# Performance work log

Hardware: AMD Instinct MI355X
Metric: run time of the kernel (lower is better)

Reference implementation:

```python
import jax, jax.numpy as jnp
import numpy as np
from jax import lax

B, ROWS, COLS, K, LATENT = 8, 1536, 16, 32, 16
EPS_REG = 0.01  # torchsort regularization_strength
BIG = 1e30


def setup_inputs() -> dict:
    key = jax.random.key(0)
    ks = jax.random.split(key, 12)
    def w(k, shape):
        return (jax.random.normal(k, shape, jnp.float32) / np.sqrt(shape[0])).astype(jnp.float32)
    return {
        "table": jax.random.uniform(ks[0], (B, ROWS, COLS), jnp.float32),
        "enc_w1": w(ks[1], (COLS, 32)), "enc_b1": 0.01 * jax.random.normal(ks[2], (32,), jnp.float32),
        "enc_w2": w(ks[3], (32, 64)),   "enc_b2": 0.01 * jax.random.normal(ks[4], (64,), jnp.float32),
        "mean_w": w(ks[5], (64, LATENT)), "mean_b": 0.01 * jax.random.normal(ks[6], (LATENT,), jnp.float32),
        "dec_w1": w(ks[7], (LATENT, 32)), "dec_b1": 0.01 * jax.random.normal(ks[8], (32,), jnp.float32),
        "dec_w2": w(ks[9], (32, COLS)),   "dec_b2": 0.01 * jax.random.normal(ks[10], (COLS,), jnp.float32),
        "labels": jax.random.randint(ks[11], (ROWS,), 0, K, jnp.int32),
        "BlockSize": 64,
        "current_epoch": 0,
        "baseline": 0,
    }


def _soft_rank_l2(s, eps):
    # Exact soft_rank (Blondel et al. / torchsort, l2 reg, ascending):
    # project s/eps onto permutahedron of (n,...,1).
    n = s.shape[0]
    x = s / eps
    perm = jnp.argsort(-x)            # descending sort
    xs = x[perm]
    w = jnp.arange(n, 0, -1, dtype=x.dtype)
    # dual = non-increasing isotonic fit of y = xs - w == -iso_inc(-(xs - w))
    y = -(xs - w)
    S = jnp.concatenate([jnp.zeros((1,), x.dtype), jnp.cumsum(y)])
    idx = jnp.arange(n)
    length = jnp.maximum(idx[None, :] - idx[:, None] + 1, 1).astype(x.dtype)
    A = (S[1:][None, :] - S[:n][:, None]) / length           # mean(y[j..k])  [j,k]
    A = jnp.where(idx[None, :] >= idx[:, None], A, BIG)
    Bm = lax.cummin(A, axis=1, reverse=True)                  # min_{k>=i} A[j,k]
    Cm = lax.cummax(Bm, axis=0)                               # max_{j<=i} ...
    iso_inc = jnp.diagonal(Cm)
    dual = -iso_inc
    primal = xs - dual
    inv = jnp.argsort(perm)
    return primal[inv]


def _forward(table, enc_w1, enc_b1, enc_w2, enc_b2, mean_w, mean_b,
             dec_w1, dec_b1, dec_w2, dec_b2, labels, BlockSize):
    b = table.shape[0]
    # VAE (autoencoder path; z = latent mean)
    h = jax.nn.relu(table @ enc_w1 + enc_b1)
    h = jax.nn.relu(h @ enc_w2 + enc_b2)
    z = h @ mean_w + mean_b                                   # [B, rows, 16]
    r = jax.nn.relu(z @ dec_w1 + dec_b1)
    recon = jax.nn.relu(r @ dec_w2 + dec_b2)
    loss = jnp.mean((recon - table) ** 2)
    # clustering scores (labels fixed from batch 0, shared across batch)
    onehot = jax.nn.one_hot(labels, K, dtype=z.dtype)         # [rows, K]
    counts = jnp.maximum(onehot.sum(0), 1.0)                  # [K]
    centers = jnp.einsum('brd,rk->bkd', z, onehot) / counts[None, :, None]
    center_data = centers[:, labels, :]                       # gather back [B, rows, 16]
    d2 = jnp.mean((z - center_data) ** 2, axis=-1)            # [B, rows]
    mn = d2.min(axis=1, keepdims=True); mx = d2.max(axis=1, keepdims=True)
    d2 = (d2 - mn) / (mx - mn)
    scores = d2 + labels.astype(z.dtype)[None, :]
    # training branch
    smn = scores.min(axis=1, keepdims=True); smx = scores.max(axis=1, keepdims=True)
    scaled = (scores - smn) / (smx - smn) * jnp.asarray(b, z.dtype)  # * len(table)
    ranks = jax.vmap(lambda s: _soft_rank_l2(s, EPS_REG))(scaled)
    rank_idx = jnp.argsort(jnp.argsort(scores, axis=1), axis=1) // BlockSize + 1
    rows = table.shape[1]
    return (ranks.reshape(b, rows, 1), rank_idx.reshape(b, rows, 1),
            scores.reshape(b, rows, 1), loss)


def reference(table, enc_w1, enc_b1, enc_w2, enc_b2, mean_w, mean_b,
              dec_w1, dec_b1, dec_w2, dec_b2, labels, BlockSize,
              current_epoch, baseline):
    return _forward(table, enc_w1, enc_b1, enc_w2, enc_b2, mean_w, mean_b,
                    dec_w1, dec_b1, dec_w2, dec_b2, labels, BlockSize)
```

## Files before the change

### kernel.cpp

```cpp
#include <hip/hip_runtime.h>

#define BATCH 8
#define ROWS 1536
#define KCLS 32
#define NTOT (BATCH*ROWS)
#define ELEMS (NTOT*16)
#define SSTRIDE 3073
#define BIGF 1.0e30f

enum : int {
  WS_Z     = 0,
  WS_X     = WS_Z + NTOT*16,
  WS_XS    = WS_X + NTOT,
  WS_S     = WS_XS + NTOT,
  WS_DESC  = WS_S + BATCH*SSTRIDE,
  WS_ASCP  = WS_DESC + NTOT,
  WS_DSCP  = WS_ASCP + 4*NTOT,
  WS_GPART = WS_DSCP + 4*NTOT,
  WS_LOSSP = WS_GPART + BATCH*96*512,
  WS_D2    = WS_LOSSP + 768,
  WS_MM    = WS_D2 + NTOT,
};
#define WS_CPART WS_GPART

#define LW1  0
#define LB1  512
#define LW2  544
#define LB2  2592
#define LMW  2656
#define LMB  3680
#define LDW1 3696
#define LDB1 4208
#define LDW2 4240
#define LDB2 4752
#define LTOT 4768

#define AX   0
#define AH1  16
#define AH2  48
#define AZ   112
#define AR1  128
#define AREC 144
#define ASTRIDE 164

#define RPB 16

template<int IN_BASE, int IN_N, int OUT_BASE, int OUT_PW, int OUT_TOT,
         int WOFF, int BOFF, bool RELU>
__device__ __forceinline__ void layerw(float* __restrict__ act,
                                       const float* __restrict__ wsh,
                                       int lrow, int fway)
{
  const int o0 = fway * OUT_PW;
  float acc[OUT_PW];
#pragma unroll
  for (int j = 0; j < OUT_PW; ++j) acc[j] = wsh[BOFF + o0 + j];

  const float4* arow = reinterpret_cast<const float4*>(&act[lrow*ASTRIDE + IN_BASE]);
#pragma unroll 2
  for (int i4 = 0; i4 < IN_N/4; ++i4) {
    float4 sv = arow[i4];
    float svx[4];
    svx[0] = sv.x; svx[1] = sv.y; svx[2] = sv.z; svx[3] = sv.w;
#pragma unroll
    for (int u = 0; u < 4; ++u) {
      const float s = svx[u];
      const float* wp = &wsh[WOFF + (i4*4 + u)*OUT_TOT + o0];
      if constexpr (OUT_PW == 1) {
        acc[0] = fmaf(s, wp[0], acc[0]);
      } else if constexpr (OUT_PW == 2) {
        float2 w = *reinterpret_cast<const float2*>(wp);
        acc[0] = fmaf(s, w.x, acc[0]);
        acc[1] = fmaf(s, w.y, acc[1]);
      } else {
#pragma unroll
        for (int q = 0; q < OUT_PW/4; ++q) {
          float4 w = reinterpret_cast<const float4*>(wp)[q];
          acc[q*4+0] = fmaf(s, w.x, acc[q*4+0]);
          acc[q*4+1] = fmaf(s, w.y, acc[q*4+1]);
          acc[q*4+2] = fmaf(s, w.z, acc[q*4+2]);
          acc[q*4+3] = fmaf(s, w.w, acc[q*4+3]);
        }
      }
    }
  }
  float* orow = &act[lrow*ASTRIDE + OUT_BASE + o0];
  if constexpr (OUT_PW == 1) {
    orow[0] = RELU ? fmaxf(acc[0], 0.f) : acc[0];
  } else if constexpr (OUT_PW == 2) {
    float2 v;
    v.x = RELU ? fmaxf(acc[0], 0.f) : acc[0];
    v.y = RELU ? fmaxf(acc[1], 0.f) : acc[1];
    *reinterpret_cast<float2*>(orow) = v;
  } else {
#pragma unroll
    for (int q = 0; q < OUT_PW/4; ++q) {
      float4 v;
      v.x = RELU ? fmaxf(acc[q*4+0], 0.f) : acc[q*4+0];
      v.y = RELU ? fmaxf(acc[q*4+1], 0.f) : acc[q*4+1];
      v.z = RELU ? fmaxf(acc[q*4+2], 0.f) : acc[q*4+2];
      v.w = RELU ? fmaxf(acc[q*4+3], 0.f) : acc[q*4+3];
      reinterpret_cast<float4*>(orow)[q] = v;
    }
  }
}

__global__ __launch_bounds__(256, 4) void k1_ae(
    const float* __restrict__ table,
    const float* __restrict__ w1, const float* __restrict__ b1,
    const float* __restrict__ w2, const float* __restrict__ b2,
    const float* __restrict__ mw, const float* __restrict__ mb,
    const float* __restrict__ dw1, const float* __restrict__ db1,
    const float* __restrict__ dw2, const float* __restrict__ db2,
    const int* __restrict__ labels,
    float* __restrict__ ws)
{
  const int tid  = threadIdx.x;
  const int lrow = tid & (RPB-1);
  const int fway = tid >> 4;
  const int blk  = blockIdx.x;
  const int b    = blk / 96;
  const int ch   = blk % 96;

  __shared__ float wsh[LTOT];
  __shared__ float act[RPB * ASTRIDE];
  __shared__ int   lbl[RPB];
  __shared__ float lred[4];

  {
    float4* d4 = reinterpret_cast<float4*>(wsh);
#define CPY(off, src, nf4) \
    { const float4* p = reinterpret_cast<const float4*>(src); \
      for (int t = tid; t < (nf4); t += 256) d4[(off)/4 + t] = p[t]; }
    CPY(LW1,  w1,  128) CPY(LB1,  b1,  8)  CPY(LW2,  w2,  512)
    CPY(LB2,  b2,  16)  CPY(LMW,  mw,  256) CPY(LMB,  mb,  4)
    CPY(LDW1, dw1, 128) CPY(LDB1, db1, 8)  CPY(LDW2, dw2, 128)
    CPY(LDB2, db2, 4)
#undef CPY
    if (tid < RPB) lbl[tid] = labels[ch * RPB + tid];
    if (tid < RPB*4) {
      const float4 v = reinterpret_cast<const float4*>(table)[blk*(RPB*4) + tid];
      reinterpret_cast<float4*>(act)[(tid >> 2)*(ASTRIDE/4) + (tid & 3)] = v;
    }
  }
  __syncthreads();

  layerw<AX,  16, AH1, 2, 32, LW1,  LB1,  true >(act, wsh, lrow, fway);
  __syncthreads();
  layerw<AH1, 32, AH2, 4, 64, LW2,  LB2,  true >(act, wsh, lrow, fway);
  __syncthreads();
  layerw<AH2, 64, AZ,  1, 16, LMW,  LMB,  false>(act, wsh, lrow, fway);
  __syncthreads();

  if (tid < RPB*4) {
    const float4 zv =
      reinterpret_cast<const float4*>(act)[(tid >> 2)*(ASTRIDE/4) + (AZ/4) + (tid & 3)];
    reinterpret_cast<float4*>(ws + WS_Z)[blk*(RPB*4) + tid] = zv;
  }

  layerw<AZ,  16, AR1, 2, 32, LDW1, LDB1, true >(act, wsh, lrow, fway);
  __syncthreads();
  layerw<AR1, 32, AREC,1, 16, LDW2, LDB2, true >(act, wsh, lrow, fway);
  __syncthreads();

  {
    const float d = act[lrow*ASTRIDE + AREC + fway] - act[lrow*ASTRIDE + AX + fway];
    float ls = d * d;
    for (int off = 32; off > 0; off >>= 1) ls += __shfl_down(ls, off);
    if ((tid & 63) == 0) lred[tid >> 6] = ls;
    __syncthreads();
    if (tid == 0) ws[WS_LOSSP + blk] = (lred[0] + lred[1]) + (lred[2] + lred[3]);
  }

  {
    float a0 = 0.f, a1 = 0.f;
    const int d0 = tid & 15, k0 = tid >> 4;
    const int k1c = k0 + 16;
#pragma unroll
    for (int rr = 0; rr < RPB; ++rr) {
      const int lb = lbl[rr];
      const float zv = act[rr*ASTRIDE + AZ + d0];
      a0 += (lb == k0)  ? zv : 0.f;
      a1 += (lb == k1c) ? zv : 0.f;
    }
    ws[WS_CPART + (b*96 + ch)*512 + tid]       = a0;
    ws[WS_CPART + (b*96 + ch)*512 + 256 + tid] = a1;
  }
}

__global__ __launch_bounds__(256) void kcd2(const int* __restrict__ labels,
                                            float* __restrict__ ws,
                                            float* __restrict__ out)
{
  const int bi = blockIdx.x;
  const int b = bi / 6, ib = bi % 6;
  const int tid = threadIdx.x;

  __shared__ int   cnt[KCLS];
  __shared__ int   lbls[256];
  __shared__ float cent[512];
  __shared__ float rmn[256], rmx[256];

  if (tid < KCLS) cnt[tid] = 0;
  __syncthreads();
#pragma unroll
  for (int c = 0; c < 6; ++c) {
    const int lb = labels[c*256 + tid];
    if (c == ib) lbls[tid] = lb;
    atomicAdd(&cnt[lb], 1);
  }
  __syncthreads();

#pragma unroll
  for (int e = tid; e < 512; e += 256) {
    float s = 0.f;
#pragma unroll 8
    for (int c = 0; c < 96; ++c) s += ws[WS_CPART + (b*96 + c)*512 + e];
    const int cn = cnt[e >> 4] > 1 ? cnt[e >> 4] : 1;
    cent[e] = s / (float)cn;
  }
  __syncthreads();

  const int r = ib*256 + tid;
  {
    const int lb = lbls[tid];
    const float4* zp = reinterpret_cast<const float4*>(ws + WS_Z + (b*ROWS + r)*16);
    const float4* cp = reinterpret_cast<const float4*>(&cent[lb*16]);
    float s = 0.f;
#pragma unroll
    for (int q = 0; q < 4; ++q) {
      float4 zv = zp[q], cv = cp[q];
      float d0 = zv.x - cv.x, d1 = zv.y - cv.y, d2_ = zv.z - cv.z, d3 = zv.w - cv.w;
      s += d0*d0 + d1*d1 + d2_*d2_ + d3*d3;
    }
    const float dv = s / 16.f;
    ws[WS_D2 + b*ROWS + r] = dv;
    rmn[tid] = dv; rmx[tid] = dv;
  }
  __syncthreads();
  for (int off = 128; off > 0; off >>= 1) {
    if (tid < off) {
      rmn[tid] = fminf(rmn[tid], rmn[tid + off]);
      rmx[tid] = fmaxf(rmx[tid], rmx[tid + off]);
    }
    __syncthreads();
  }
  if (tid == 0) {
    ws[WS_MM + bi*2]     = rmn[0];
    ws[WS_MM + bi*2 + 1] = rmx[0];
  }

  if (bi == 0) {
    __syncthreads();
    rmn[tid] = ws[WS_LOSSP + tid] + ws[WS_LOSSP + 256 + tid] + ws[WS_LOSSP + 512 + tid];
    __syncthreads();
    for (int off = 128; off > 0; off >>= 1) {
      if (tid < off) rmn[tid] += rmn[tid + off];
      __syncthreads();
    }
    if (tid == 0) out[3*NTOT] = rmn[0] / (float)ELEMS;
  }
}

__global__ __launch_bounds__(256) void kcount(const int* __restrict__ labels,
                                              float* __restrict__ ws,
                                              float* __restrict__ out)
{
  const int bi = blockIdx.x;
  const int jb = bi & 3, rb = (bi >> 2) % 6, b = bi / 24;
  const int tid = threadIdx.x;

  alignas(16) __shared__ float s_l[ROWS];
  alignas(16) __shared__ float x_l[ROWS];
  __shared__ float rmn[256], rmx[256];

  float mn = 3.0e38f, mx = -3.0e38f;
#pragma unroll
  for (int c = 0; c < 6; ++c) {
    mn = fminf(mn, ws[WS_MM + (b*6 + c)*2]);
    mx = fmaxf(mx, ws[WS_MM + (b*6 + c)*2 + 1]);
  }

  float tmn = 3.0e38f, tmx = -3.0e38f;
#pragma unroll
  for (int c = 0; c < 6; ++c) {
    const int r = c*256 + tid;
    const float sc = (ws[WS_D2 + b*ROWS + r] - mn) / (mx - mn) + (float)labels[r];
    s_l[r] = sc;
    if (jb == 0 && c == rb) out[2*NTOT + b*ROWS + r] = sc;
    tmn = fminf(tmn, sc); tmx = fmaxf(tmx, sc);
  }
  rmn[tid] = tmn; rmx[tid] = tmx;
  __syncthreads();
  for (int off = 128; off > 0; off >>= 1) {
    if (tid < off) {
      rmn[tid] = fminf(rmn[tid], rmn[tid + off]);
      rmx[tid] = fmaxf(rmx[tid], rmx[tid + off]);
    }
    __syncthreads();
  }
  const float smn = rmn[0], smx = rmx[0];

#pragma unroll
  for (int c = 0; c < 6; ++c) {
    const int r = c*256 + tid;
    const float scl = (s_l[r] - smn) / (smx - smn) * 8.0f;
    const float xv = scl / 0.01f;
    x_l[r] = xv;
    if (jb == 0 && c == rb) ws[WS_X + b*ROWS + r] = xv;
  }
  __syncthreads();

  const int r0 = rb*256 + tid;
  const float si = s_l[r0], xi = x_l[r0];
  int asc = 0, dsc = 0;
  const int j0 = jb*384;
  const float4* s4p = reinterpret_cast<const float4*>(&s_l[j0]);
  const float4* x4p = reinterpret_cast<const float4*>(&x_l[j0]);
#pragma unroll 4
  for (int kk = 0; kk < 96; ++kk) {
    const float4 s4 = s4p[kk];
    const float4 x4 = x4p[kk];
    const int j = j0 + kk*4;
    asc += (s4.x < si || (s4.x == si && j   < r0)) ? 1 : 0;
    asc += (s4.y < si || (s4.y == si && j+1 < r0)) ? 1 : 0;
    asc += (s4.z < si || (s4.z == si && j+2 < r0)) ? 1 : 0;
    asc += (s4.w < si || (s4.w == si && j+3 < r0)) ? 1 : 0;
    dsc += (x4.x > xi || (x4.x == xi && j   < r0)) ? 1 : 0;
    dsc += (x4.y > xi || (x4.y == xi && j+1 < r0)) ? 1 : 0;
    dsc += (x4.z > xi || (x4.z == xi && j+2 < r0)) ? 1 : 0;
    dsc += (x4.w > xi || (x4.w == xi && j+3 < r0)) ? 1 : 0;
  }
  int* wsi = reinterpret_cast<int*>(ws);
  wsi[WS_ASCP + jb*NTOT + b*ROWS + r0] = asc;
  wsi[WS_DSCP + jb*NTOT + b*ROWS + r0] = dsc;
}

__global__ __launch_bounds__(256) void k67(const int* __restrict__ bsp,
                                           float* __restrict__ ws,
                                           float* __restrict__ out)
{
  const int b = blockIdx.x, tid = threadIdx.x;
  const int lane = tid & 63, wav = tid >> 6;
  __shared__ float xs_l[ROWS];
  __shared__ float wtot[4];
  const int* wsi = reinterpret_cast<const int*>(ws);
  int* wsw = reinterpret_cast<int*>(ws);
  const int BS = *bsp;
#pragma unroll
  for (int c = 0; c < 6; ++c) {
    const int r = c*256 + tid;
    const int idx = b*ROWS + r;
    int asc = 0, dsc = 0;
#pragma unroll
    for (int jb = 0; jb < 4; ++jb) {
      asc += wsi[WS_ASCP + jb*NTOT + idx];
      dsc += wsi[WS_DSCP + jb*NTOT + idx];
    }
    out[NTOT + idx] = (float)(asc / BS + 1);
    wsw[WS_DESC + idx] = dsc;
    xs_l[dsc] = ws[WS_X + idx];
  }
  __syncthreads();
  const int base = tid * 6;
  float y[6], own = 0.f;
#pragma unroll
  for (int u = 0; u < 6; ++u) {
    ws[WS_XS + b*ROWS + base + u] = xs_l[base + u];
    y[u] = (float)(ROWS - (base + u)) - xs_l[base + u];
    own += y[u];
  }
  float v = own;
#pragma unroll
  for (int d = 1; d < 64; d <<= 1) {
    float o = __shfl_up(v, d);
    if (lane >= d) v += o;
  }
  if (lane == 63) wtot[wav] = v;
  __syncthreads();
  float wpre = 0.f;
  for (int w = 0; w < wav; ++w) wpre += wtot[w];
  float run = wpre + (v - own);
  float* S = ws + WS_S + b*SSTRIDE;
#pragma unroll
  for (int u = 0; u < 6; ++u) { S[base + u] = run; run += y[u]; }
  if (tid == 255) S[ROWS] = run;
#pragma unroll
  for (int u = 0; u < 6; ++u) S[ROWS + 1 + tid*6 + u] = BIGF;
}

__global__ __launch_bounds__(256) void k8a(float* __restrict__ ws)
{
  const int bi = blockIdx.x;
  const int c = bi & 7, ib = (bi >> 3) % 6, b = bi / 48;
  const int tid = threadIdx.x;
  __shared__ float Sseg[448];
  __shared__ float invl[192];
  const float* S = ws + WS_S + b*SSTRIDE;
  const int ibase = ib*256;
  const int segbase = ibase + c*192 + 1;
  Sseg[tid] = S[segbase + tid];
  if (tid < 192) {
    Sseg[256 + tid] = S[segbase + 256 + tid];
    invl[tid] = 1.0f / (float)(c*192 + tid + 1);
  }
  __syncthreads();
  const int i = ibase + tid;
  const float Si = S[i];
  float gm = 3.0e38f;
#pragma unroll 8
  for (int k = 0; k < 192; ++k)
    gm = fminf(gm, (Sseg[tid + k] - Si) * invl[k]);
  ws[WS_GPART + (b*8 + c)*ROWS + i] = gm;
}

__global__ __launch_bounds__(768) void k8b(float* __restrict__ ws,
                                           float* __restrict__ out)
{
  const int b = blockIdx.x, tid = threadIdx.x;
  const int lane = tid & 63, wav = tid >> 6;
  __shared__ float g[ROWS];
  __shared__ float wtot[12];
  for (int t = tid; t < ROWS; t += 768) {
    float gm = 3.0e38f;
#pragma unroll
    for (int c = 0; c < 8; ++c)
      gm = fminf(gm, ws[WS_GPART + (b*8 + c)*ROWS + t]);
    g[t] = gm;
  }
  __syncthreads();
  const float a = g[2*tid], cc = g[2*tid + 1];
  float v = fmaxf(a, cc);
#pragma unroll
  for (int d = 1; d < 64; d <<= 1) {
    float o = __shfl_up(v, d);
    if (lane >= d) v = fmaxf(v, o);
  }
  if (lane == 63) wtot[wav] = v;
  __syncthreads();
  float wpre = -3.0e38f;
  for (int w = 0; w < wav; ++w) wpre = fmaxf(wpre, wtot[w]);
  float lex = __shfl_up(v, 1);
  if (lane == 0) lex = -3.0e38f;
  const float excl = fmaxf(wpre, lex);
  const float i0 = fmaxf(excl, a);
  const float i1 = fmaxf(i0, cc);
  g[2*tid] = i0; g[2*tid + 1] = i1;
  __syncthreads();
  const float* xs = ws + WS_XS + b*ROWS;
  const int* desc = reinterpret_cast<const int*>(ws) + WS_DESC + b*ROWS;
  for (int t = tid; t < ROWS; t += 768) {
    const int dr = desc[t];
    out[b*ROWS + t] = xs[dr] + g[dr];
  }
}

extern "C" void kernel_launch(void* const* d_in, const int* in_sizes, int n_in,
                              void* d_out, int out_size, void* d_ws, size_t ws_size,
                              hipStream_t stream) {
  const float* table = (const float*)d_in[0];
  const float* w1  = (const float*)d_in[1];
  const float* b1  = (const float*)d_in[2];
  const float* w2  = (const float*)d_in[3];
  const float* b2  = (const float*)d_in[4];
  const float* mw  = (const float*)d_in[5];
  const float* mb  = (const float*)d_in[6];
  const float* dw1 = (const float*)d_in[7];
  const float* db1 = (const float*)d_in[8];
  const float* dw2 = (const float*)d_in[9];
  const float* db2 = (const float*)d_in[10];
  const int* labels = (const int*)d_in[11];
  const int* bsp    = (const int*)d_in[12];
  float* out = (float*)d_out;
  float* ws  = (float*)d_ws;

  k1_ae<<<768, 256, 0, stream>>>(table, w1, b1, w2, b2, mw, mb, dw1, db1, dw2, db2, labels, ws);
  kcd2<<<48, 256, 0, stream>>>(labels, ws, out);
  kcount<<<192, 256, 0, stream>>>(labels, ws, out);
  k67<<<8, 256, 0, stream>>>(bsp, ws, out);
  k8a<<<384, 256, 0, stream>>>(ws);
  k8b<<<8, 768, 0, stream>>>(ws, out);
}
```

Baseline: 69.99 us.

## Compute per-batch scores and scaled ranks once in a 1024-thread block kernel

```diff
diff --git a/kernel.cpp b/kernel.cpp
--- a/kernel.cpp
+++ b/kernel.cpp
@@ -18,8 +18,6 @@
   WS_DSCP  = WS_ASCP + 4*NTOT,
   WS_GPART = WS_DSCP + 4*NTOT,
   WS_LOSSP = WS_GPART + BATCH*96*512,
-  WS_D2    = WS_LOSSP + 768,
-  WS_MM    = WS_D2 + NTOT,
 };
 #define WS_CPART WS_GPART
 
@@ -188,83 +186,117 @@
   }
 }
 
-__global__ __launch_bounds__(256) void kcd2(const int* __restrict__ labels,
-                                            float* __restrict__ ws,
-                                            float* __restrict__ out)
-{
-  const int bi = blockIdx.x;
-  const int b = bi / 6, ib = bi % 6;
+__global__ __launch_bounds__(1024) void kmid8(const int* __restrict__ labels,
+                                              float* __restrict__ ws,
+                                              float* __restrict__ out)
+{
+  const int b = blockIdx.x;
   const int tid = threadIdx.x;
-
-  __shared__ int   cnt[KCLS];
-  __shared__ int   lbls[256];
-  __shared__ float cent[512];
-  __shared__ float rmn[256], rmx[256];
+  const int lane = tid & 63, wav = tid >> 6;
+
+  __shared__ int cnt[KCLS];
+  alignas(16) __shared__ float cent[512];
+  alignas(16) __shared__ float part[1024];
+  __shared__ float wr1[16], wr2[16];
 
   if (tid < KCLS) cnt[tid] = 0;
   __syncthreads();
-#pragma unroll
-  for (int c = 0; c < 6; ++c) {
-    const int lb = labels[c*256 + tid];
-    if (c == ib) lbls[tid] = lb;
-    atomicAdd(&cnt[lb], 1);
-  }
-  __syncthreads();
-
-#pragma unroll
-  for (int e = tid; e < 512; e += 256) {
+  const int lb1 = labels[tid];
+  const int lb2 = (tid < 512) ? labels[1024 + tid] : 0;
+  atomicAdd(&cnt[lb1], 1);
+  if (tid < 512) atomicAdd(&cnt[lb2], 1);
+
+  {
+    const int e = tid & 511, g = tid >> 9;
+    const float* cp = ws + WS_CPART + (b*96 + g*48)*512 + e;
     float s = 0.f;
 #pragma unroll 8
-    for (int c = 0; c < 96; ++c) s += ws[WS_CPART + (b*96 + c)*512 + e];
-    const int cn = cnt[e >> 4] > 1 ? cnt[e >> 4] : 1;
-    cent[e] = s / (float)cn;
-  }
-  __syncthreads();
-
-  const int r = ib*256 + tid;
-  {
-    const int lb = lbls[tid];
+    for (int c = 0; c < 48; ++c) s += cp[c*512];
+    part[tid] = s;
+  }
+  __syncthreads();
+  if (tid < 512) {
+    const int cn = cnt[tid >> 4] > 1 ? cnt[tid >> 4] : 1;
+    cent[tid] = (part[tid] + part[tid + 512]) / (float)cn;
+  }
+
+  if (b == 0) {
+    float ls = (tid < 768) ? ws[WS_LOSSP + tid] : 0.f;
+    for (int off = 32; off > 0; off >>= 1) ls += __shfl_down(ls, off);
+    if (lane == 0) wr1[wav] = ls;
+  }
+  __syncthreads();
+  if (b == 0 && tid == 0) {
+    float L = 0.f;
+#pragma unroll
+    for (int w = 0; w < 16; ++w) L += wr1[w];
+    out[3*NTOT] = L / (float)ELEMS;
+  }
+
+  auto d2row = [&](int r, int lb) -> float {
     const float4* zp = reinterpret_cast<const float4*>(ws + WS_Z + (b*ROWS + r)*16);
-    const float4* cp = reinterpret_cast<const float4*>(&cent[lb*16]);
+    const float4* cq = reinterpret_cast<const float4*>(&cent[lb*16]);
     float s = 0.f;
 #pragma unroll
     for (int q = 0; q < 4; ++q) {
-      float4 zv = zp[q], cv = cp[q];
+      float4 zv = zp[q], cv = cq[q];
       float d0 = zv.x - cv.x, d1 = zv.y - cv.y, d2_ = zv.z - cv.z, d3 = zv.w - cv.w;
       s += d0*d0 + d1*d1 + d2_*d2_ + d3*d3;
     }
-    const float dv = s / 16.f;
-    ws[WS_D2 + b*ROWS + r] = dv;
-    rmn[tid] = dv; rmx[tid] = dv;
-  }
-  __syncthreads();
-  for (int off = 128; off > 0; off >>= 1) {
-    if (tid < off) {
-      rmn[tid] = fminf(rmn[tid], rmn[tid + off]);
-      rmx[tid] = fmaxf(rmx[tid], rmx[tid + off]);
-    }
-    __syncthreads();
-  }
-  if (tid == 0) {
-    ws[WS_MM + bi*2]     = rmn[0];
-    ws[WS_MM + bi*2 + 1] = rmx[0];
-  }
-
-  if (bi == 0) {
-    __syncthreads();
-    rmn[tid] = ws[WS_LOSSP + tid] + ws[WS_LOSSP + 256 + tid] + ws[WS_LOSSP + 512 + tid];
-    __syncthreads();
-    for (int off = 128; off > 0; off >>= 1) {
-      if (tid < off) rmn[tid] += rmn[tid + off];
-      __syncthreads();
-    }
-    if (tid == 0) out[3*NTOT] = rmn[0] / (float)ELEMS;
-  }
-}
-
-__global__ __launch_bounds__(256) void kcount(const int* __restrict__ labels,
-                                              float* __restrict__ ws,
-                                              float* __restrict__ out)
+    return s / 16.f;
+  };
+  const float dv1 = d2row(tid, lb1);
+  const float dv2 = (tid < 512) ? d2row(1024 + tid, lb2) : 0.f;
+
+  {
+    float mn = (tid < 512) ? fminf(dv1, dv2) : dv1;
+    float mx = (tid < 512) ? fmaxf(dv1, dv2) : dv1;
+    for (int off = 32; off > 0; off >>= 1) {
+      mn = fminf(mn, __shfl_down(mn, off));
+      mx = fmaxf(mx, __shfl_down(mx, off));
+    }
+    if (lane == 0) { wr1[wav] = mn; wr2[wav] = mx; }
+  }
+  __syncthreads();
+  float mn = 3.0e38f, mx = -3.0e38f;
+#pragma unroll
+  for (int w = 0; w < 16; ++w) {
+    mn = fminf(mn, wr1[w]); mx = fmaxf(mx, wr2[w]);
+  }
+  __syncthreads();
+
+  const float sc1 = (dv1 - mn) / (mx - mn) + (float)lb1;
+  const float sc2 = (tid < 512) ? (dv2 - mn) / (mx - mn) + (float)lb2 : 0.f;
+  out[2*NTOT + b*ROWS + tid] = sc1;
+  if (tid < 512) out[2*NTOT + b*ROWS + 1024 + tid] = sc2;
+  {
+    float smn = (tid < 512) ? fminf(sc1, sc2) : sc1;
+    float smx = (tid < 512) ? fmaxf(sc1, sc2) : sc1;
+    for (int off = 32; off > 0; off >>= 1) {
+      smn = fminf(smn, __shfl_down(smn, off));
+      smx = fmaxf(smx, __shfl_down(smx, off));
+    }
+    if (lane == 0) { wr1[wav] = smn; wr2[wav] = smx; }
+  }
+  __syncthreads();
+  float smn = 3.0e38f, smx = -3.0e38f;
+#pragma unroll
+  for (int w = 0; w < 16; ++w) {
+    smn = fminf(smn, wr1[w]); smx = fmaxf(smx, wr2[w]);
+  }
+
+  {
+    const float x1 = (sc1 - smn) / (smx - smn) * 8.0f / 0.01f;
+    ws[WS_X + b*ROWS + tid] = x1;
+    if (tid < 512) {
+      const float x2 = (sc2 - smn) / (smx - smn) * 8.0f / 0.01f;
+      ws[WS_X + b*ROWS + 1024 + tid] = x2;
+    }
+  }
+}
+
+__global__ __launch_bounds__(256) void kcount(float* __restrict__ ws,
+                                              const float* __restrict__ out)
 {
   const int bi = blockIdx.x;
   const int jb = bi & 3, rb = (bi >> 2) % 6, b = bi / 24;
@@ -272,42 +304,12 @@
 
   alignas(16) __shared__ float s_l[ROWS];
   alignas(16) __shared__ float x_l[ROWS];
-  __shared__ float rmn[256], rmx[256];
-
-  float mn = 3.0e38f, mx = -3.0e38f;
-#pragma unroll
-  for (int c = 0; c < 6; ++c) {
-    mn = fminf(mn, ws[WS_MM + (b*6 + c)*2]);
-    mx = fmaxf(mx, ws[WS_MM + (b*6 + c)*2 + 1]);
-  }
-
-  float tmn = 3.0e38f, tmx = -3.0e38f;
+
 #pragma unroll
   for (int c = 0; c < 6; ++c) {
     const int r = c*256 + tid;
-    const float sc = (ws[WS_D2 + b*ROWS + r] - mn) / (mx - mn) + (float)labels[r];
-    s_l[r] = sc;
-    if (jb == 0 && c == rb) out[2*NTOT + b*ROWS + r] = sc;
-    tmn = fminf(tmn, sc); tmx = fmaxf(tmx, sc);
-  }
-  rmn[tid] = tmn; rmx[tid] = tmx;
-  __syncthreads();
-  for (int off = 128; off > 0; off >>= 1) {
-    if (tid < off) {
-      rmn[tid] = fminf(rmn[tid], rmn[tid + off]);
-      rmx[tid] = fmaxf(rmx[tid], rmx[tid + off]);
-    }
-    __syncthreads();
-  }
-  const float smn = rmn[0], smx = rmx[0];
-
-#pragma unroll
-  for (int c = 0; c < 6; ++c) {
-    const int r = c*256 + tid;
-    const float scl = (s_l[r] - smn) / (smx - smn) * 8.0f;
-    const float xv = scl / 0.01f;
-    x_l[r] = xv;
-    if (jb == 0 && c == rb) ws[WS_X + b*ROWS + r] = xv;
+    s_l[r] = out[2*NTOT + b*ROWS + r];
+    x_l[r] = ws[WS_X + b*ROWS + r];
   }
   __syncthreads();
 
@@ -475,8 +477,8 @@
   float* ws  = (float*)d_ws;
 
   k1_ae<<<768, 256, 0, stream>>>(table, w1, b1, w2, b2, mw, mb, dw1, db1, dw2, db2, labels, ws);
-  kcd2<<<48, 256, 0, stream>>>(labels, ws, out);
-  kcount<<<192, 256, 0, stream>>>(labels, ws, out);
+  kmid8<<<8, 1024, 0, stream>>>(labels, ws, out);
+  kcount<<<192, 256, 0, stream>>>(ws, out);
   k67<<<8, 256, 0, stream>>>(bsp, ws, out);
   k8a<<<384, 256, 0, stream>>>(ws);
   k8b<<<8, 768, 0, stream>>>(ws, out);
```

Measured after the change: 61.93 us. 1.13x faster.

## Split centroid reduction into parallel kernel and derive descending ranks from scores

Applied to the files above, without the earlier changes.

```diff
diff --git a/kernel.cpp b/kernel.cpp
--- a/kernel.cpp
+++ b/kernel.cpp
@@ -10,8 +10,7 @@
 
 enum : int {
   WS_Z     = 0,
-  WS_X     = WS_Z + NTOT*16,
-  WS_XS    = WS_X + NTOT,
+  WS_XS    = WS_Z + NTOT*16,
   WS_S     = WS_XS + NTOT,
   WS_DESC  = WS_S + BATCH*SSTRIDE,
   WS_ASCP  = WS_DESC + NTOT,
@@ -20,6 +19,8 @@
   WS_LOSSP = WS_GPART + BATCH*96*512,
   WS_D2    = WS_LOSSP + 768,
   WS_MM    = WS_D2 + NTOT,
+  WS_CPAR2 = WS_MM + 96,
+  WS_CNT   = WS_CPAR2 + BATCH*8*512,
 };
 #define WS_CPART WS_GPART
 
@@ -188,55 +189,80 @@
   }
 }
 
-__global__ __launch_bounds__(256) void kcd2(const int* __restrict__ labels,
+__global__ __launch_bounds__(512) void kcen(const int* __restrict__ labels,
                                             float* __restrict__ ws,
                                             float* __restrict__ out)
+{
+  const int bi = blockIdx.x;
+  const int b = bi >> 3, g = bi & 7;
+  const int tid = threadIdx.x;
+
+  const float* cp = ws + WS_CPART + (b*96 + g*12)*512 + tid;
+  float s = 0.f;
+#pragma unroll
+  for (int c = 0; c < 12; ++c) s += cp[c*512];
+  ws[WS_CPAR2 + (b*8 + g)*512 + tid] = s;
+
+  if (bi == 0) {
+    __shared__ int icnt[KCLS];
+    __shared__ float red[512];
+    if (tid < KCLS) icnt[tid] = 0;
+    __syncthreads();
+    atomicAdd(&icnt[labels[tid]], 1);
+    atomicAdd(&icnt[labels[512 + tid]], 1);
+    atomicAdd(&icnt[labels[1024 + tid]], 1);
+    red[tid] = ws[WS_LOSSP + tid] + ((tid < 256) ? ws[WS_LOSSP + 512 + tid] : 0.f);
+    __syncthreads();
+    for (int off = 256; off > 0; off >>= 1) {
+      if (tid < off) red[tid] += red[tid + off];
+      __syncthreads();
+    }
+    if (tid == 0) out[3*NTOT] = red[0] / (float)ELEMS;
+    if (tid < KCLS) reinterpret_cast<int*>(ws)[WS_CNT + tid] = icnt[tid];
+  }
+}
+
+__global__ __launch_bounds__(256) void kd2(const int* __restrict__ labels,
+                                           float* __restrict__ ws)
 {
   const int bi = blockIdx.x;
   const int b = bi / 6, ib = bi % 6;
   const int tid = threadIdx.x;
 
-  __shared__ int   cnt[KCLS];
-  __shared__ int   lbls[256];
   __shared__ float cent[512];
   __shared__ float rmn[256], rmx[256];
-
-  if (tid < KCLS) cnt[tid] = 0;
-  __syncthreads();
-#pragma unroll
-  for (int c = 0; c < 6; ++c) {
-    const int lb = labels[c*256 + tid];
-    if (c == ib) lbls[tid] = lb;
-    atomicAdd(&cnt[lb], 1);
-  }
-  __syncthreads();
-
-#pragma unroll
-  for (int e = tid; e < 512; e += 256) {
-    float s = 0.f;
-#pragma unroll 8
-    for (int c = 0; c < 96; ++c) s += ws[WS_CPART + (b*96 + c)*512 + e];
-    const int cn = cnt[e >> 4] > 1 ? cnt[e >> 4] : 1;
-    cent[e] = s / (float)cn;
+  __shared__ int ci[KCLS];
+
+  if (tid < KCLS) ci[tid] = reinterpret_cast<const int*>(ws)[WS_CNT + tid];
+  float s1 = 0.f, s2 = 0.f;
+#pragma unroll
+  for (int g = 0; g < 8; ++g) {
+    s1 += ws[WS_CPAR2 + (b*8 + g)*512 + tid];
+    s2 += ws[WS_CPAR2 + (b*8 + g)*512 + 256 + tid];
+  }
+  __syncthreads();
+  {
+    int cn1 = ci[tid >> 4];         cn1 = cn1 > 1 ? cn1 : 1;
+    int cn2 = ci[(tid + 256) >> 4]; cn2 = cn2 > 1 ? cn2 : 1;
+    cent[tid]       = s1 / (float)cn1;
+    cent[tid + 256] = s2 / (float)cn2;
   }
   __syncthreads();
 
   const int r = ib*256 + tid;
-  {
-    const int lb = lbls[tid];
-    const float4* zp = reinterpret_cast<const float4*>(ws + WS_Z + (b*ROWS + r)*16);
-    const float4* cp = reinterpret_cast<const float4*>(&cent[lb*16]);
-    float s = 0.f;
-#pragma unroll
-    for (int q = 0; q < 4; ++q) {
-      float4 zv = zp[q], cv = cp[q];
-      float d0 = zv.x - cv.x, d1 = zv.y - cv.y, d2_ = zv.z - cv.z, d3 = zv.w - cv.w;
-      s += d0*d0 + d1*d1 + d2_*d2_ + d3*d3;
-    }
-    const float dv = s / 16.f;
-    ws[WS_D2 + b*ROWS + r] = dv;
-    rmn[tid] = dv; rmx[tid] = dv;
-  }
+  const int lb = labels[r];
+  const float4* zp = reinterpret_cast<const float4*>(ws + WS_Z + (b*ROWS + r)*16);
+  const float4* cq = reinterpret_cast<const float4*>(&cent[lb*16]);
+  float s = 0.f;
+#pragma unroll
+  for (int q = 0; q < 4; ++q) {
+    float4 zv = zp[q], cv = cq[q];
+    float d0 = zv.x - cv.x, d1 = zv.y - cv.y, d2_ = zv.z - cv.z, d3 = zv.w - cv.w;
+    s += d0*d0 + d1*d1 + d2_*d2_ + d3*d3;
+  }
+  const float dv = s / 16.f;
+  ws[WS_D2 + b*ROWS + r] = dv;
+  rmn[tid] = dv; rmx[tid] = dv;
   __syncthreads();
   for (int off = 128; off > 0; off >>= 1) {
     if (tid < off) {
@@ -249,17 +275,6 @@
     ws[WS_MM + bi*2]     = rmn[0];
     ws[WS_MM + bi*2 + 1] = rmx[0];
   }
-
-  if (bi == 0) {
-    __syncthreads();
-    rmn[tid] = ws[WS_LOSSP + tid] + ws[WS_LOSSP + 256 + tid] + ws[WS_LOSSP + 512 + tid];
-    __syncthreads();
-    for (int off = 128; off > 0; off >>= 1) {
-      if (tid < off) rmn[tid] += rmn[tid + off];
-      __syncthreads();
-    }
-    if (tid == 0) out[3*NTOT] = rmn[0] / (float)ELEMS;
-  }
 }
 
 __global__ __launch_bounds__(256) void kcount(const int* __restrict__ labels,
@@ -271,8 +286,6 @@
   const int tid = threadIdx.x;
 
   alignas(16) __shared__ float s_l[ROWS];
-  alignas(16) __shared__ float x_l[ROWS];
-  __shared__ float rmn[256], rmx[256];
 
   float mn = 3.0e38f, mx = -3.0e38f;
 #pragma unroll
@@ -281,13 +294,73 @@
     mx = fmaxf(mx, ws[WS_MM + (b*6 + c)*2 + 1]);
   }
 
-  float tmn = 3.0e38f, tmx = -3.0e38f;
 #pragma unroll
   for (int c = 0; c < 6; ++c) {
     const int r = c*256 + tid;
     const float sc = (ws[WS_D2 + b*ROWS + r] - mn) / (mx - mn) + (float)labels[r];
     s_l[r] = sc;
     if (jb == 0 && c == rb) out[2*NTOT + b*ROWS + r] = sc;
+  }
+  __syncthreads();
+
+  const int r0 = rb*256 + tid;
+  const float si = s_l[r0];
+  int asc = 0, dsc = 0;
+  const int j0 = jb*384;
+  const float4* s4p = reinterpret_cast<const float4*>(&s_l[j0]);
+#pragma unroll 4
+  for (int kk = 0; kk < 96; ++kk) {
+    const float4 s4 = s4p[kk];
+    const int j = j0 + kk*4;
+    const bool t0 = (s4.x == si && j   < r0);
+    const bool t1 = (s4.y == si && j+1 < r0);
+    const bool t2 = (s4.z == si && j+2 < r0);
+    const bool t3 = (s4.w == si && j+3 < r0);
+    asc += (s4.x < si || t0) ? 1 : 0;
+    asc += (s4.y < si || t1) ? 1 : 0;
+    asc += (s4.z < si || t2) ? 1 : 0;
+    asc += (s4.w < si || t3) ? 1 : 0;
+    dsc += (s4.x > si || t0) ? 1 : 0;
+    dsc += (s4.y > si || t1) ? 1 : 0;
+    dsc += (s4.z > si || t2) ? 1 : 0;
+    dsc += (s4.w > si || t3) ? 1 : 0;
+  }
+  int* wsi = reinterpret_cast<int*>(ws);
+  wsi[WS_ASCP + jb*NTOT + b*ROWS + r0] = asc;
+  wsi[WS_DSCP + jb*NTOT + b*ROWS + r0] = dsc;
+}
+
+__global__ __launch_bounds__(256) void k67(const int* __restrict__ bsp,
+                                           float* __restrict__ ws,
+                                           float* __restrict__ out)
+{
+  const int b = blockIdx.x, tid = threadIdx.x;
+  const int lane = tid & 63, wav = tid >> 6;
+  __shared__ float xs_l[ROWS];
+  __shared__ float rmn[256], rmx[256];
+  __shared__ float wtot[4];
+  const int* wsi = reinterpret_cast<const int*>(ws);
+  int* wsw = reinterpret_cast<int*>(ws);
+  const int BS = *bsp;
+
+  int dscv[6];
+  float sv[6];
+  float tmn = 3.0e38f, tmx = -3.0e38f;
+#pragma unroll
+  for (int c = 0; c < 6; ++c) {
+    const int r = c*256 + tid;
+    const int idx = b*ROWS + r;
+    int asc = 0, dsc = 0;
+#pragma unroll
+    for (int jb = 0; jb < 4; ++jb) {
+      asc += wsi[WS_ASCP + jb*NTOT + idx];
+      dsc += wsi[WS_DSCP + jb*NTOT + idx];
+    }
+    out[NTOT + idx] = (float)(asc / BS + 1);
+    wsw[WS_DESC + idx] = dsc;
+    dscv[c] = dsc;
+    const float sc = out[2*NTOT + idx];
+    sv[c] = sc;
     tmn = fminf(tmn, sc); tmx = fmaxf(tmx, sc);
   }
   rmn[tid] = tmn; rmx[tid] = tmx;
@@ -300,68 +373,15 @@
     __syncthreads();
   }
   const float smn = rmn[0], smx = rmx[0];
+  __syncthreads();
 
 #pragma unroll
   for (int c = 0; c < 6; ++c) {
-    const int r = c*256 + tid;
-    const float scl = (s_l[r] - smn) / (smx - smn) * 8.0f;
-    const float xv = scl / 0.01f;
-    x_l[r] = xv;
-    if (jb == 0 && c == rb) ws[WS_X + b*ROWS + r] = xv;
-  }
-  __syncthreads();
-
-  const int r0 = rb*256 + tid;
-  const float si = s_l[r0], xi = x_l[r0];
-  int asc = 0, dsc = 0;
-  const int j0 = jb*384;
-  const float4* s4p = reinterpret_cast<const float4*>(&s_l[j0]);
-  const float4* x4p = reinterpret_cast<const float4*>(&x_l[j0]);
-#pragma unroll 4
-  for (int kk = 0; kk < 96; ++kk) {
-    const float4 s4 = s4p[kk];
-    const float4 x4 = x4p[kk];
-    const int j = j0 + kk*4;
-    asc += (s4.x < si || (s4.x == si && j   < r0)) ? 1 : 0;
-    asc += (s4.y < si || (s4.y == si && j+1 < r0)) ? 1 : 0;
-    asc += (s4.z < si || (s4.z == si && j+2 < r0)) ? 1 : 0;
-    asc += (s4.w < si || (s4.w == si && j+3 < r0)) ? 1 : 0;
-    dsc += (x4.x > xi || (x4.x == xi && j   < r0)) ? 1 : 0;
-    dsc += (x4.y > xi || (x4.y == xi && j+1 < r0)) ? 1 : 0;
-    dsc += (x4.z > xi || (x4.z == xi && j+2 < r0)) ? 1 : 0;
-    dsc += (x4.w > xi || (x4.w == xi && j+3 < r0)) ? 1 : 0;
-  }
-  int* wsi = reinterpret_cast<int*>(ws);
-  wsi[WS_ASCP + jb*NTOT + b*ROWS + r0] = asc;
-  wsi[WS_DSCP + jb*NTOT + b*ROWS + r0] = dsc;
-}
-
-__global__ __launch_bounds__(256) void k67(const int* __restrict__ bsp,
-                                           float* __restrict__ ws,
-                                           float* __restrict__ out)
-{
-  const int b = blockIdx.x, tid = threadIdx.x;
-  const int lane = tid & 63, wav = tid >> 6;
-  __shared__ float xs_l[ROWS];
-  __shared__ float wtot[4];
-  const int* wsi = reinterpret_cast<const int*>(ws);
-  int* wsw = reinterpret_cast<int*>(ws);
-  const int BS = *bsp;
-#pragma unroll
-  for (int c = 0; c < 6; ++c) {
-    const int r = c*256 + tid;
-    const int idx = b*ROWS + r;
-    int asc = 0, dsc = 0;
-#pragma unroll
-    for (int jb = 0; jb < 4; ++jb) {
-      asc += wsi[WS_ASCP + jb*NTOT + idx];
-      dsc += wsi[WS_DSCP + jb*NTOT + idx];
-    }
-    out[NTOT + idx] = (float)(asc / BS + 1);
-    wsw[WS_DESC + idx] = dsc;
-    xs_l[dsc] = ws[WS_X + idx];
-  }
-  __syncthreads();
+    const float scl = (sv[c] - smn) / (smx - smn) * 8.0f;
+    xs_l[dscv[c]] = scl / 0.01f;
+  }
+  __syncthreads();
+
   const int base = tid * 6;
   float y[6], own = 0.f;
 #pragma unroll
@@ -475,7 +495,8 @@
   float* ws  = (float*)d_ws;
 
   k1_ae<<<768, 256, 0, stream>>>(table, w1, b1, w2, b2, mw, mb, dw1, db1, dw2, db2, labels, ws);
-  kcd2<<<48, 256, 0, stream>>>(labels, ws, out);
+  kcen<<<64, 512, 0, stream>>>(labels, ws, out);
+  kd2<<<48, 256, 0, stream>>>(labels, ws);
   kcount<<<192, 256, 0, stream>>>(labels, ws, out);
   k67<<<8, 256, 0, stream>>>(bsp, ws, out);
   k8a<<<384, 256, 0, stream>>>(ws);
```

Result: faster. 59.49 us (-15.0%).
